# Kernel optimization log

Hardware: AMD Instinct MI355X
Metric: run time of the kernel (lower is better)

The kernel has to match this reference:

```python
import jax, jax.numpy as jnp
import numpy as np

D = 256
H = 256
B = 128
T = 512


def _init_cell(key, input_size, hidden_size):
    K = 1.0 / np.sqrt(hidden_size)
    k1, k2, k3, k4 = jax.random.split(key, 4)
    u = lambda k, shape: jax.random.uniform(k, shape, jnp.float32, -K, K)
    return (u(k1, (3 * hidden_size, input_size)),
            u(k2, (3 * hidden_size, hidden_size)),
            u(k3, (3 * hidden_size,)),
            u(k4, (3 * hidden_size,)))


def setup_inputs() -> dict:
    key = jax.random.key(0)
    kx, kf, kb = jax.random.split(key, 3)
    x = jax.random.normal(kx, (B, T, D), dtype=jnp.float32)
    w_ih_fw, w_hh_fw, b_ih_fw, b_hh_fw = _init_cell(kf, D, H)
    w_ih_bw, w_hh_bw, b_ih_bw, b_hh_bw = _init_cell(kb, D, H)
    return {
        "x": x,
        "w_ih_fw": w_ih_fw, "w_hh_fw": w_hh_fw, "b_ih_fw": b_ih_fw, "b_hh_fw": b_hh_fw,
        "w_ih_bw": w_ih_bw, "w_hh_bw": w_hh_bw, "b_ih_bw": b_ih_bw, "b_hh_bw": b_hh_bw,
    }


def _gru_scan(x_tbd, w_ih, w_hh, b_ih, b_hh):
    # x_tbd: [T, B, D]; returns outputs [T, B, H] and final h [B, H]
    h0 = jnp.zeros((x_tbd.shape[1], H), dtype=x_tbd.dtype)

    def step(h, x_t):
        xT = x_t @ w_ih.T + b_ih          # [B, 3H]
        hT = h @ w_hh.T + b_hh            # [B, 3H]
        s = jax.nn.sigmoid(xT + hT)
        r = s[:, :H]
        z = s[:, H:2 * H]
        n = jnp.tanh(xT[:, 2 * H:] + r * hT[:, 2 * H:])
        h_new = (1.0 - z) * n + z * h
        return h_new, h_new

    h_last, outs = jax.lax.scan(step, h0, x_tbd)
    return outs, h_last


def reference(x, w_ih_fw, w_hh_fw, b_ih_fw, b_hh_fw,
              w_ih_bw, w_hh_bw, b_ih_bw, b_hh_bw):
    x_tbd = jnp.swapaxes(x, 0, 1)                         # [T, B, D]
    outs_fw, h_fw = _gru_scan(x_tbd, w_ih_fw, w_hh_fw, b_ih_fw, b_hh_fw)
    outs_bw_rev, h_bw = _gru_scan(x_tbd[::-1], w_ih_bw, w_hh_bw, b_ih_bw, b_hh_bw)
    outs_bw = outs_bw_rev[::-1]
    outputs = jnp.concatenate([outs_fw, outs_bw], axis=-1)  # [T, B, 2H]
    outputs = jnp.swapaxes(outputs, 0, 1)                   # [B, T, 2H]
    return outputs, h_fw, h_bw
```

## Files before the change

kernel.cpp:

```cpp
#include <hip/hip_runtime.h>
#include <stdint.h>
#include <stddef.h>

#define T_ 512
#define B_ 128
#define D_ 256
#define H_ 256
#define NR 768
#define OUT_MAIN 33554432ull
#define XT_STRIDE 12288
#define HOUT_OFF 8192
#define HB 280

typedef __attribute__((ext_vector_type(4))) float f32x4;
typedef __attribute__((ext_vector_type(8))) short s16x8;
typedef __attribute__((ext_vector_type(4))) uint32_t u32x4;
typedef __attribute__((ext_vector_type(2))) uint32_t u32x2;

__device__ __forceinline__ unsigned short f2bf(float f) {
    union { float f; uint32_t u; } v; v.f = f;
    return (unsigned short)((v.u + 0x7FFFu + ((v.u >> 16) & 1u)) >> 16);
}
__device__ __forceinline__ float lo16(uint32_t w) {
    union { uint32_t u; float f; } v; v.u = w << 16; return v.f;
}
__device__ __forceinline__ float hi16(uint32_t w) {
    union { uint32_t u; float f; } v; v.u = w & 0xffff0000u; return v.f;
}
__device__ __forceinline__ uint32_t cvtpk(float a, float b) {
    uint32_t r;
    asm("v_cvt_pk_bf16_f32 %0, %1, %2" : "=v"(r) : "v"(a), "v"(b));
    return r;
}
__device__ __forceinline__ float sigm(float x) {
    return __builtin_amdgcn_rcpf(1.f + __expf(-x));
}
__device__ __forceinline__ float tanh_(float x) {
    float e = __expf(2.f * x);
    return 1.f - 2.f * __builtin_amdgcn_rcpf(e + 1.f);
}
__device__ __forceinline__ s16x8 pack8(const float* f) {
    union { s16x8 v; unsigned short u[8]; } p;
#pragma unroll
    for (int i = 0; i < 8; ++i) p.u[i] = f2bf(f[i]);
    return p.v;
}

__global__ void k_convert(const float* __restrict__ wf, const float* __restrict__ wb,
                          unsigned short* __restrict__ dst) {
    int i = blockIdx.x * blockDim.x + threadIdx.x;
    const int n = NR * D_;
    if (i < n) dst[i] = f2bf(wf[i]);
    else if (i < 2 * n) dst[i] = f2bf(wb[i - n]);
}

__global__ __launch_bounds__(512, 2) void k_xgemm(
    const float* __restrict__ x, const unsigned short* __restrict__ wbf,
    const float* __restrict__ bih_f, const float* __restrict__ bhh_f,
    const float* __restrict__ bih_b, const float* __restrict__ bhh_b,
    unsigned short* __restrict__ XT)
{
    __shared__ __align__(16) unsigned short lds_a[32 * 72];
    __shared__ __align__(16) unsigned short xt_l[2 * XT_STRIDE];
    const int tid = threadIdx.x, lane = tid & 63, wn = tid >> 6;
    const int t = blockIdx.x;
    const int dir = blockIdx.y >> 2, q2 = blockIdx.y & 3;

    f32x4 acc[2][6];
#pragma unroll
    for (int m = 0; m < 2; ++m)
#pragma unroll
        for (int n = 0; n < 6; ++n) acc[m][n] = (f32x4){0.f, 0.f, 0.f, 0.f};

    for (int kb = 0; kb < 4; ++kb) {
        if (kb) __syncthreads();
        {
            int row = tid >> 4, c4 = (tid & 15) * 4;
            const float* src = x + ((size_t)(q2 * 32 + row) * T_ + t) * D_ + kb * 64 + c4;
            f32x4 f = *(const f32x4*)src;
            u32x2 p = { cvtpk(f[0], f[1]), cvtpk(f[2], f[3]) };
            *(u32x2*)&lds_a[row * 72 + c4] = p;
        }
        __syncthreads();
#pragma unroll
        for (int kt = 0; kt < 2; ++kt) {
            s16x8 av[2];
#pragma unroll
            for (int mt = 0; mt < 2; ++mt) {
                int r = mt * 16 + (lane & 15);
                av[mt] = *(const s16x8*)&lds_a[r * 72 + kt * 32 + (lane >> 4) * 8];
            }
#pragma unroll
            for (int nt = 0; nt < 6; ++nt) {
                int c = dir * NR + wn * 96 + nt * 16 + (lane & 15);
                s16x8 bv = *(const s16x8*)(wbf + (size_t)c * D_ + kb * 64 + kt * 32 + (lane >> 4) * 8);
#pragma unroll
                for (int mt = 0; mt < 2; ++mt)
                    acc[mt][nt] = __builtin_amdgcn_mfma_f32_16x16x32_bf16(av[mt], bv, acc[mt][nt], 0, 0, 0);
            }
        }
    }
    const float* bih = dir ? bih_b : bih_f;
    const float* bhh = dir ? bhh_b : bhh_f;
    __syncthreads();
#pragma unroll
    for (int nt = 0; nt < 6; ++nt) {
        const int cw = wn * 96 + nt * 16 + (lane & 15);
        const int gate = cw >> 8, j = cw & 255;
        const int jt = (j >> 4) & 1;
        const int rtid = (j >> 5) * 64 + ((lane >> 4) << 4) + (j & 15);
        float bias = bih[cw] + (cw < 512 ? bhh[cw] : 0.f);
#pragma unroll
        for (int mt = 0; mt < 2; ++mt) {
#pragma unroll
            for (int q = 0; q < 4; ++q) {
                int v = (jt * 4 + q) * 3 + gate;
                xt_l[mt * XT_STRIDE + rtid * 24 + v] = f2bf(acc[mt][nt][q] + bias);
            }
        }
    }
    __syncthreads();
#pragma unroll
    for (int half = 0; half < 2; ++half) {
        size_t base = ((size_t)(dir * 8 + q2 * 2 + half) * T_ + t) * XT_STRIDE;
#pragma unroll
        for (int k = 0; k < 3; ++k)
            *(u32x4*)(XT + base + (size_t)tid * 24 + k * 8)
                = *(const u32x4*)&xt_l[half * XT_STRIDE + tid * 24 + k * 8];
    }
}

template<int P>
__device__ __forceinline__ void gru_step(
    int s, int dir, int tid, int lane, int wid,
    const unsigned short* __restrict__ XTw, unsigned short* __restrict__ XTw_mut,
    unsigned short* hb, const s16x8 (&fB)[6][8], float bhn0, float bhn1,
    u32x4 (&CUR)[3], u32x4 (&NXT)[3], float (&hreg)[8])
{
    const int t  = dir ? (T_ - 1 - s) : s;
    const int sn = (s < T_ - 1) ? s + 1 : s;
    const int tn = dir ? (T_ - 1 - sn) : sn;
    {
        const u32x4* p = (const u32x4*)(XTw + (size_t)tn * XT_STRIDE) + (size_t)tid * 3;
        NXT[0] = p[0]; NXT[1] = p[1]; NXT[2] = p[2];
    }
    const unsigned short* hr = hb + P * (16 * HB);
    unsigned short*       hw = hb + (P ^ 1) * (16 * HB);

    s16x8 a[8];
#pragma unroll
    for (int k0 = 0; k0 < 8; ++k0)
        a[k0] = *(const s16x8*)&hr[(lane & 15) * HB + k0 * 32 + (lane >> 4) * 8];

    f32x4 acc[6];
#pragma unroll
    for (int n = 0; n < 6; ++n) acc[n] = (f32x4){0.f, 0.f, 0.f, 0.f};
#pragma unroll
    for (int k0 = 0; k0 < 8; ++k0) {
#pragma unroll
        for (int nt = 0; nt < 6; ++nt)
            acc[nt] = __builtin_amdgcn_mfma_f32_16x16x32_bf16(a[k0], fB[nt][k0], acc[nt], 0, 0, 0);
    }

    float hn[8];
#pragma unroll
    for (int jt = 0; jt < 2; ++jt) {
        const float bn = jt ? bhn1 : bhn0;
#pragma unroll
        for (int q = 0; q < 4; ++q) {
            const int idx = jt * 4 + q;
            const int v = idx * 3;
            uint32_t w0 = CUR[(v)     >> 3][((v)     >> 1) & 3];
            uint32_t w1 = CUR[(v + 1) >> 3][((v + 1) >> 1) & 3];
            uint32_t w2 = CUR[(v + 2) >> 3][((v + 2) >> 1) & 3];
            float xr = (v & 1)       ? hi16(w0) : lo16(w0);
            float xz = ((v + 1) & 1) ? hi16(w1) : lo16(w1);
            float xn = ((v + 2) & 1) ? hi16(w2) : lo16(w2);
            float rg = sigm(acc[jt][q] + xr);
            float zg = sigm(acc[2 + jt][q] + xz);
            float ng = tanh_(xn + rg * (acc[4 + jt][q] + bn));
            hn[idx] = ng + zg * (hreg[idx] - ng);
            hreg[idx] = hn[idx];
        }
    }
    u32x4 pk;
#pragma unroll
    for (int k = 0; k < 4; ++k) pk[k] = cvtpk(hn[2 * k], hn[2 * k + 1]);
#pragma unroll
    for (int k = 0; k < 4; ++k) {
        const int i0 = 2 * k, i1 = 2 * k + 1;
        const int j = 32 * wid + (i0 >> 2) * 16 + (lane & 15);
        const int r0 = (lane >> 4) * 4 + (i0 & 3);
        hw[r0 * HB + j]       = (unsigned short)pk[k];
        hw[(r0 + 1) * HB + j] = (unsigned short)(pk[k] >> 16);
        (void)i1;
    }
    *((u32x4*)(XTw_mut + (size_t)t * XT_STRIDE + HOUT_OFF) + tid) = pk;

    __builtin_amdgcn_sched_barrier(0);
    asm volatile("s_waitcnt lgkmcnt(0)");
    __builtin_amdgcn_s_barrier();
    __builtin_amdgcn_sched_barrier(0);
}

__global__ __launch_bounds__(512, 2) void k_recur(
    const float* __restrict__ whh_f, const float* __restrict__ whh_b,
    const float* __restrict__ bhh_f, const float* __restrict__ bhh_b,
    unsigned short* __restrict__ XT)
{
    __shared__ __align__(16) unsigned short hb[2 * 16 * HB];
    const int tid = threadIdx.x, lane = tid & 63, wid = tid >> 6;
    const int bid = blockIdx.x;
    const int dir = bid >> 3;
    const float* whh = dir ? whh_b : whh_f;
    const float* bhh = dir ? bhh_b : bhh_f;

    s16x8 fB[6][8];
#pragma unroll
    for (int g = 0; g < 3; ++g) {
#pragma unroll
        for (int half = 0; half < 2; ++half) {
            int nt = 2 * g + half;
            int cb = g * 256 + 32 * wid + half * 16;
#pragma unroll
            for (int k0 = 0; k0 < 8; ++k0) {
                const float* sp = whh + (size_t)(cb + (lane & 15)) * H_ + k0 * 32 + (lane >> 4) * 8;
                float fv[8];
                *(f32x4*)&fv[0] = *(const f32x4*)(sp);
                *(f32x4*)&fv[4] = *(const f32x4*)(sp + 4);
                fB[nt][k0] = pack8(fv);
            }
        }
    }
    const float bhn0 = bhh[512 + 32 * wid + (lane & 15)];
    const float bhn1 = bhh[512 + 32 * wid + 16 + (lane & 15)];

    for (int i = tid; i < 16 * HB / 2; i += 512) ((uint32_t*)hb)[i] = 0;
    __syncthreads();

    unsigned short* XTw = XT + (size_t)bid * T_ * XT_STRIDE;
    u32x4 XA[3], XB[3];
    float hreg[8];
#pragma unroll
    for (int i = 0; i < 8; ++i) hreg[i] = 0.f;
    {
        const int t0 = dir ? (T_ - 1) : 0;
        const u32x4* p = (const u32x4*)(XTw + (size_t)t0 * XT_STRIDE) + (size_t)tid * 3;
        XA[0] = p[0]; XA[1] = p[1]; XA[2] = p[2];
    }
#pragma unroll 1
    for (int s = 0; s < T_; s += 2) {
        gru_step<0>(s,     dir, tid, lane, wid, XTw, XTw, hb, fB, bhn0, bhn1, XA, XB, hreg);
        gru_step<1>(s + 1, dir, tid, lane, wid, XTw, XTw, hb, fB, bhn0, bhn1, XB, XA, hreg);
    }
}

__global__ __launch_bounds__(512) void k_scatter(const unsigned short* __restrict__ XT,
                                                 float* __restrict__ out) {
    const int tid = threadIdx.x, lane = tid & 63, wid = tid >> 6;
    const int t = blockIdx.x & 511, wg = blockIdx.x >> 9;
    const int dir = wg >> 3, b0 = (wg & 7) * 16;
    u32x4 v = *((const u32x4*)(XT + ((size_t)wg * T_ + t) * XT_STRIDE + HOUT_OFF) + tid);
    const bool last = (t == (dir ? 0 : T_ - 1));
#pragma unroll
    for (int k = 0; k < 4; ++k) {
#pragma unroll
        for (int half = 0; half < 2; ++half) {
            const int idx = 2 * k + half;
            const int q = idx & 3, jt = idx >> 2;
            const int row = (lane >> 4) * 4 + q;
            const int j = 32 * wid + jt * 16 + (lane & 15);
            const int b = b0 + row;
            float val = half ? hi16(v[k]) : lo16(v[k]);
            out[((size_t)b * T_ + t) * 512 + (size_t)dir * 256 + j] = val;
            if (last)
                out[OUT_MAIN + (size_t)dir * B_ * H_ + (size_t)b * H_ + j] = val;
        }
    }
}

extern "C" void kernel_launch(void* const* d_in, const int* in_sizes, int n_in,
                              void* d_out, int out_size, void* d_ws, size_t ws_size,
                              hipStream_t stream) {
    const float* x     = (const float*)d_in[0];
    const float* wih_f = (const float*)d_in[1];
    const float* whh_f = (const float*)d_in[2];
    const float* bih_f = (const float*)d_in[3];
    const float* bhh_f = (const float*)d_in[4];
    const float* wih_b = (const float*)d_in[5];
    const float* whh_b = (const float*)d_in[6];
    const float* bih_b = (const float*)d_in[7];
    const float* bhh_b = (const float*)d_in[8];
    float* out = (float*)d_out;

    unsigned short* wbf = (unsigned short*)d_ws;
    unsigned short* XT  = (unsigned short*)((char*)d_ws + 786432);

    k_convert<<<dim3(768), dim3(512), 0, stream>>>(wih_f, wih_b, wbf);
    k_xgemm<<<dim3(512, 8), dim3(512), 0, stream>>>(x, wbf, bih_f, bhh_f, bih_b, bhh_b, XT);
    k_recur<<<dim3(16), dim3(512), 0, stream>>>(whh_f, whh_b, bhh_f, bhh_b, XT);
    k_scatter<<<dim3(16 * 512), dim3(512), 0, stream>>>(XT, out);
}
```

Baseline: 1.728 ms.

## Split GRU recurrence across 16 waves and fuse output scatter into it

The recurrent kernel now runs 1024 threads per block, so each wave owns 16 hidden columns instead of 32. That halves the serial MFMA chain and gate math per wave on each timestep, and the xgemm staging layout is reordered to match. The separate scatter kernel and the bf16 hidden-state staging in the workspace are removed: fp32 outputs and the final states are stored to the output directly from the recurrence. In exchange, every step now issues scattered global stores inside the latency-critical loop, and 16 waves synchronise at each barrier instead of 8.

```diff
diff --git a/kernel.cpp b/kernel.cpp
--- a/kernel.cpp
+++ b/kernel.cpp
@@ -9,7 +9,6 @@
 #define NR 768
 #define OUT_MAIN 33554432ull
 #define XT_STRIDE 12288
-#define HOUT_OFF 8192
 #define HB 280
 
 typedef __attribute__((ext_vector_type(4))) float f32x4;
@@ -107,15 +106,14 @@
     for (int nt = 0; nt < 6; ++nt) {
         const int cw = wn * 96 + nt * 16 + (lane & 15);
         const int gate = cw >> 8, j = cw & 255;
-        const int jt = (j >> 4) & 1;
-        const int rtid = (j >> 5) * 64 + ((lane >> 4) << 4) + (j & 15);
+        const int tid_r = (j >> 4) * 64 + ((lane >> 4) << 4) + (j & 15);
         float bias = bih[cw] + (cw < 512 ? bhh[cw] : 0.f);
 #pragma unroll
         for (int mt = 0; mt < 2; ++mt) {
 #pragma unroll
             for (int q = 0; q < 4; ++q) {
-                int v = (jt * 4 + q) * 3 + gate;
-                xt_l[mt * XT_STRIDE + rtid * 24 + v] = f2bf(acc[mt][nt][q] + bias);
+                int v = q * 3 + gate;
+                xt_l[mt * XT_STRIDE + tid_r * 12 + v] = f2bf(acc[mt][nt][q] + bias);
             }
         }
     }
@@ -132,16 +130,16 @@
 
 template<int P>
 __device__ __forceinline__ void gru_step(
-    int s, int dir, int tid, int lane, int wid,
-    const unsigned short* __restrict__ XTw, unsigned short* __restrict__ XTw_mut,
-    unsigned short* hb, const s16x8 (&fB)[6][8], float bhn0, float bhn1,
-    u32x4 (&CUR)[3], u32x4 (&NXT)[3], float (&hreg)[8])
+    int s, int dir, int b0, int tid, int lane, int wid,
+    const unsigned short* __restrict__ XTw, float* __restrict__ out,
+    unsigned short* hb, const s16x8 (&fB)[3][8], float bn,
+    u32x2 (&CUR)[3], u32x2 (&NXT)[3], float (&hreg)[4])
 {
     const int t  = dir ? (T_ - 1 - s) : s;
     const int sn = (s < T_ - 1) ? s + 1 : s;
     const int tn = dir ? (T_ - 1 - sn) : sn;
     {
-        const u32x4* p = (const u32x4*)(XTw + (size_t)tn * XT_STRIDE) + (size_t)tid * 3;
+        const u32x2* p = (const u32x2*)(XTw + (size_t)tn * XT_STRIDE) + (size_t)tid * 3;
         NXT[0] = p[0]; NXT[1] = p[1]; NXT[2] = p[2];
     }
     const unsigned short* hr = hb + P * (16 * HB);
@@ -152,130 +150,97 @@
     for (int k0 = 0; k0 < 8; ++k0)
         a[k0] = *(const s16x8*)&hr[(lane & 15) * HB + k0 * 32 + (lane >> 4) * 8];
 
-    f32x4 acc[6];
-#pragma unroll
-    for (int n = 0; n < 6; ++n) acc[n] = (f32x4){0.f, 0.f, 0.f, 0.f};
+    f32x4 acc[3];
+#pragma unroll
+    for (int g = 0; g < 3; ++g) acc[g] = (f32x4){0.f, 0.f, 0.f, 0.f};
 #pragma unroll
     for (int k0 = 0; k0 < 8; ++k0) {
 #pragma unroll
-        for (int nt = 0; nt < 6; ++nt)
-            acc[nt] = __builtin_amdgcn_mfma_f32_16x16x32_bf16(a[k0], fB[nt][k0], acc[nt], 0, 0, 0);
-    }
-
-    float hn[8];
-#pragma unroll
-    for (int jt = 0; jt < 2; ++jt) {
-        const float bn = jt ? bhn1 : bhn0;
+        for (int g = 0; g < 3; ++g)
+            acc[g] = __builtin_amdgcn_mfma_f32_16x16x32_bf16(a[k0], fB[g][k0], acc[g], 0, 0, 0);
+    }
+
+    const int j = 16 * wid + (lane & 15);
+    float hn[4];
+#pragma unroll
+    for (int q = 0; q < 4; ++q) {
+        const int v = q * 3;
+        uint32_t w0 = CUR[(v)     >> 2][((v)     >> 1) & 1];
+        uint32_t w1 = CUR[(v + 1) >> 2][((v + 1) >> 1) & 1];
+        uint32_t w2 = CUR[(v + 2) >> 2][((v + 2) >> 1) & 1];
+        float xr = (v & 1)       ? hi16(w0) : lo16(w0);
+        float xz = ((v + 1) & 1) ? hi16(w1) : lo16(w1);
+        float xn = ((v + 2) & 1) ? hi16(w2) : lo16(w2);
+        float rg = sigm(acc[0][q] + xr);
+        float zg = sigm(acc[1][q] + xz);
+        float ng = tanh_(xn + rg * (acc[2][q] + bn));
+        hn[q] = ng + zg * (hreg[q] - ng);
+        hreg[q] = hn[q];
+    }
+#pragma unroll
+    for (int q = 0; q < 4; ++q) {
+        const int row = (lane >> 4) * 4 + q;
+        hw[row * HB + j] = (unsigned short)cvtpk(hn[q], hn[q]);
+        out[((size_t)(b0 + row) << 18) + ((size_t)t << 9) + (size_t)dir * 256 + j] = hn[q];
+    }
+    if (s == T_ - 1) {
 #pragma unroll
         for (int q = 0; q < 4; ++q) {
-            const int idx = jt * 4 + q;
-            const int v = idx * 3;
-            uint32_t w0 = CUR[(v)     >> 3][((v)     >> 1) & 3];
-            uint32_t w1 = CUR[(v + 1) >> 3][((v + 1) >> 1) & 3];
-            uint32_t w2 = CUR[(v + 2) >> 3][((v + 2) >> 1) & 3];
-            float xr = (v & 1)       ? hi16(w0) : lo16(w0);
-            float xz = ((v + 1) & 1) ? hi16(w1) : lo16(w1);
-            float xn = ((v + 2) & 1) ? hi16(w2) : lo16(w2);
-            float rg = sigm(acc[jt][q] + xr);
-            float zg = sigm(acc[2 + jt][q] + xz);
-            float ng = tanh_(xn + rg * (acc[4 + jt][q] + bn));
-            hn[idx] = ng + zg * (hreg[idx] - ng);
-            hreg[idx] = hn[idx];
-        }
-    }
-    u32x4 pk;
-#pragma unroll
-    for (int k = 0; k < 4; ++k) pk[k] = cvtpk(hn[2 * k], hn[2 * k + 1]);
-#pragma unroll
-    for (int k = 0; k < 4; ++k) {
-        const int i0 = 2 * k, i1 = 2 * k + 1;
-        const int j = 32 * wid + (i0 >> 2) * 16 + (lane & 15);
-        const int r0 = (lane >> 4) * 4 + (i0 & 3);
-        hw[r0 * HB + j]       = (unsigned short)pk[k];
-        hw[(r0 + 1) * HB + j] = (unsigned short)(pk[k] >> 16);
-        (void)i1;
-    }
-    *((u32x4*)(XTw_mut + (size_t)t * XT_STRIDE + HOUT_OFF) + tid) = pk;
-
+            const int row = (lane >> 4) * 4 + q;
+            out[OUT_MAIN + (size_t)dir * B_ * H_ + (size_t)(b0 + row) * H_ + j] = hn[q];
+        }
+    }
     __builtin_amdgcn_sched_barrier(0);
     asm volatile("s_waitcnt lgkmcnt(0)");
     __builtin_amdgcn_s_barrier();
     __builtin_amdgcn_sched_barrier(0);
 }
 
-__global__ __launch_bounds__(512, 2) void k_recur(
+__global__ __launch_bounds__(1024, 4) void k_recur(
     const float* __restrict__ whh_f, const float* __restrict__ whh_b,
     const float* __restrict__ bhh_f, const float* __restrict__ bhh_b,
-    unsigned short* __restrict__ XT)
+    const unsigned short* __restrict__ XT,
+    float* __restrict__ out)
 {
     __shared__ __align__(16) unsigned short hb[2 * 16 * HB];
     const int tid = threadIdx.x, lane = tid & 63, wid = tid >> 6;
     const int bid = blockIdx.x;
-    const int dir = bid >> 3;
+    const int dir = bid >> 3, b0 = (bid & 7) * 16;
     const float* whh = dir ? whh_b : whh_f;
     const float* bhh = dir ? bhh_b : bhh_f;
 
-    s16x8 fB[6][8];
+    const int j = 16 * wid + (lane & 15);
+    s16x8 fB[3][8];
 #pragma unroll
     for (int g = 0; g < 3; ++g) {
 #pragma unroll
-        for (int half = 0; half < 2; ++half) {
-            int nt = 2 * g + half;
-            int cb = g * 256 + 32 * wid + half * 16;
-#pragma unroll
-            for (int k0 = 0; k0 < 8; ++k0) {
-                const float* sp = whh + (size_t)(cb + (lane & 15)) * H_ + k0 * 32 + (lane >> 4) * 8;
-                float fv[8];
-                *(f32x4*)&fv[0] = *(const f32x4*)(sp);
-                *(f32x4*)&fv[4] = *(const f32x4*)(sp + 4);
-                fB[nt][k0] = pack8(fv);
-            }
-        }
-    }
-    const float bhn0 = bhh[512 + 32 * wid + (lane & 15)];
-    const float bhn1 = bhh[512 + 32 * wid + 16 + (lane & 15)];
-
-    for (int i = tid; i < 16 * HB / 2; i += 512) ((uint32_t*)hb)[i] = 0;
+        for (int k0 = 0; k0 < 8; ++k0) {
+            const float* sp = whh + (size_t)(g * 256 + j) * H_ + k0 * 32 + (lane >> 4) * 8;
+            float fv[8];
+            *(f32x4*)&fv[0] = *(const f32x4*)(sp);
+            *(f32x4*)&fv[4] = *(const f32x4*)(sp + 4);
+            fB[g][k0] = pack8(fv);
+        }
+    }
+    const float bn = bhh[512 + j];
+
+    for (int i = tid; i < 16 * HB / 2; i += 1024) ((uint32_t*)hb)[i] = 0;
     __syncthreads();
 
-    unsigned short* XTw = XT + (size_t)bid * T_ * XT_STRIDE;
-    u32x4 XA[3], XB[3];
-    float hreg[8];
-#pragma unroll
-    for (int i = 0; i < 8; ++i) hreg[i] = 0.f;
+    const unsigned short* XTw = XT + (size_t)bid * T_ * XT_STRIDE;
+    u32x2 XA[3], XB[3];
+    float hreg[4];
+#pragma unroll
+    for (int i = 0; i < 4; ++i) hreg[i] = 0.f;
     {
         const int t0 = dir ? (T_ - 1) : 0;
-        const u32x4* p = (const u32x4*)(XTw + (size_t)t0 * XT_STRIDE) + (size_t)tid * 3;
+        const u32x2* p = (const u32x2*)(XTw + (size_t)t0 * XT_STRIDE) + (size_t)tid * 3;
         XA[0] = p[0]; XA[1] = p[1]; XA[2] = p[2];
     }
 #pragma unroll 1
     for (int s = 0; s < T_; s += 2) {
-        gru_step<0>(s,     dir, tid, lane, wid, XTw, XTw, hb, fB, bhn0, bhn1, XA, XB, hreg);
-        gru_step<1>(s + 1, dir, tid, lane, wid, XTw, XTw, hb, fB, bhn0, bhn1, XB, XA, hreg);
-    }
-}
-
-__global__ __launch_bounds__(512) void k_scatter(const unsigned short* __restrict__ XT,
-                                                 float* __restrict__ out) {
-    const int tid = threadIdx.x, lane = tid & 63, wid = tid >> 6;
-    const int t = blockIdx.x & 511, wg = blockIdx.x >> 9;
-    const int dir = wg >> 3, b0 = (wg & 7) * 16;
-    u32x4 v = *((const u32x4*)(XT + ((size_t)wg * T_ + t) * XT_STRIDE + HOUT_OFF) + tid);
-    const bool last = (t == (dir ? 0 : T_ - 1));
-#pragma unroll
-    for (int k = 0; k < 4; ++k) {
-#pragma unroll
-        for (int half = 0; half < 2; ++half) {
-            const int idx = 2 * k + half;
-            const int q = idx & 3, jt = idx >> 2;
-            const int row = (lane >> 4) * 4 + q;
-            const int j = 32 * wid + jt * 16 + (lane & 15);
-            const int b = b0 + row;
-            float val = half ? hi16(v[k]) : lo16(v[k]);
-            out[((size_t)b * T_ + t) * 512 + (size_t)dir * 256 + j] = val;
-            if (last)
-                out[OUT_MAIN + (size_t)dir * B_ * H_ + (size_t)b * H_ + j] = val;
-        }
+        gru_step<0>(s,     dir, b0, tid, lane, wid, XTw, out, hb, fB, bn, XA, XB, hreg);
+        gru_step<1>(s + 1, dir, b0, tid, lane, wid, XTw, out, hb, fB, bn, XB, XA, hreg);
     }
 }
 
@@ -298,6 +263,5 @@
 
     k_convert<<<dim3(768), dim3(512), 0, stream>>>(wih_f, wih_b, wbf);
     k_xgemm<<<dim3(512, 8), dim3(512), 0, stream>>>(x, wbf, bih_f, bhh_f, bih_b, bhh_b, XT);
-    k_recur<<<dim3(16), dim3(512), 0, stream>>>(whh_f, whh_b, bhh_f, bhh_b, XT);
-    k_scatter<<<dim3(16 * 512), dim3(512), 0, stream>>>(XT, out);
-}
+    k_recur<<<dim3(16), dim3(1024), 0, stream>>>(whh_f, whh_b, bhh_f, bhh_b, XT, out);
+}
```

Result: slower. 2.105 ms (+21.8%).
